# Kernel tuning notes

Measured on AMD Instinct MI355X. Metric: run time of the kernel, lower is better.

The kernel has to match this reference:

```python
import jax, jax.numpy as jnp
import numpy as np


def setup_inputs() -> dict:
    key = jax.random.key(0)
    ks = jax.random.split(key, 8)
    B, T, Hh, Ww, C = 4, 1024, 64, 64, 256
    f = lambda k, s: jax.random.normal(k, s, dtype=jnp.float32)
    return {
        "query_row": f(ks[0], (B, T, C)),
        "query_col": f(ks[1], (B, T, C)),
        "key_row": f(ks[2], (B, Hh, Ww, C)),
        "key_col": f(ks[3], (B, Hh, Ww, C)),
        "value": f(ks[4], (B, Hh, Ww, C)),
        "in_proj_weight": f(ks[5], (5 * C, C)) * 0.02,
        "in_proj_bias": jnp.zeros((5 * C,), jnp.float32),
        "out_w": f(ks[6], (C, C)) * 0.02,
        "out_b": jnp.zeros((C,), jnp.float32),
        "lin_w": f(ks[7], (C, C)) * 0.02,
        "lin_b": jnp.zeros((C,), jnp.float32),
        "num_heads": 8,
    }


def reference(query_row, query_col, key_row, key_col, value,
              in_proj_weight, in_proj_bias, out_w, out_b, lin_w, lin_b,
              num_heads):
    B, T, C = query_row.shape
    Hh, Ww = key_col.shape[1], key_row.shape[2]
    nh = num_heads
    hd = C // nh
    scaling = float(hd) ** -0.5
    W5 = in_proj_weight.reshape(5, C, C)
    b5 = in_proj_bias.reshape(5, C)
    # pooled sigmoid gate over value: AdaptiveAvgPool2d(1) == mean over H,W
    v_avg = jax.nn.sigmoid(value.mean(axis=(1, 2)) @ lin_w.T + lin_b)  # [B, C]
    q_row = (query_row @ W5[0].T + b5[0]) * scaling                    # [B, T, C]
    q_col = (query_col @ W5[1].T + b5[1]) * scaling                    # [B, T, C]
    k_row = (key_row @ W5[2].T + b5[2]).mean(axis=1) * v_avg[:, None, :]  # [B, W, C]
    k_col = (key_col @ W5[3].T + b5[3]).mean(axis=2) * v_avg[:, None, :]  # [B, H, C]
    v = value @ W5[4].T + b5[4]                                        # [B, H, W, C]
    # split heads (C -> nh*hd, same layout as torch view)
    qr = q_row.reshape(B, T, nh, hd)
    qc = q_col.reshape(B, T, nh, hd)
    kr = k_row.reshape(B, Ww, nh, hd)
    kc = k_col.reshape(B, Hh, nh, hd)
    vh = v.reshape(B, Hh, Ww, nh, hd)
    attn_row = jax.nn.softmax(jnp.einsum('btnd,bwnd->bntw', qr, kr), axis=-1)  # [B,nh,T,W]
    attn_col = jax.nn.softmax(jnp.einsum('btnd,bhnd->bnth', qc, kc), axis=-1)  # [B,nh,T,H]
    # column attention over rows of v, then row attention combines
    out_col = jnp.einsum('bnth,bhwnd->bntwd', attn_col, vh)            # [B,nh,T,W,hd]
    out = jnp.einsum('bntw,bntwd->btnd', attn_row, out_col).reshape(B, T, C)
    attn_output = (out @ out_w.T + out_b).transpose(1, 0, 2)           # [T, B, C]
    # head-averaged outer-product attention map [T, B, H, W]
    grid = jnp.einsum('bntw,bnth->tbhw', attn_row, attn_col) / nh
    return attn_output, grid
```

## Files before the change

kernel.cpp:

```cpp
#include <hip/hip_runtime.h>
#include <hip/hip_bf16.h>
#include <math.h>

using bf16x8 = __attribute__((ext_vector_type(8))) short;
using f32x4  = __attribute__((ext_vector_type(4))) float;
using s16x4  = __attribute__((ext_vector_type(4))) short;

static __device__ __forceinline__ float sigmoidf_(float x){ return 1.f/(1.f+__expf(-x)); }
static __device__ __forceinline__ unsigned f2bfu(float f){
  union { float f; unsigned u; } x; x.f = f;
  return (x.u + 0x7FFFu + ((x.u>>16)&1u)) >> 16;
}
static __device__ __forceinline__ short f2bf(float f){ return (short)f2bfu(f); }
static __device__ __forceinline__ unsigned pack2bf(float lo, float hi){
  __hip_bfloat162 h = __float22bfloat162_rn(make_float2(lo, hi));
  unsigned r; __builtin_memcpy(&r, &h, 4);
  return r;
}
static __device__ __forceinline__ float b2f_lo(unsigned u){ union{unsigned u; float f;}x; x.u = u<<16; return x.f; }
static __device__ __forceinline__ float b2f_hi(unsigned u){ union{unsigned u; float f;}x; x.u = u & 0xFFFF0000u; return x.f; }

__device__ __forceinline__ void mfma_body(short* As, short* Bs,
    const float* __restrict__ X, const float* __restrict__ Wm,
    const float* __restrict__ bias, float* __restrict__ Y,
    int bxm, int bxn, float scale, int mode){
  int tid = threadIdx.x;
  int m0 = bxm*128, n0 = bxn*128;
  int l = tid&63, wid = tid>>6, lo16 = l&15, g = l>>4;
  int wm = wid>>1, wn = wid&1;
  f32x4 acc[4][4] = {};
  int srow = tid>>1, skq = (tid&1)*32;
  size_t arow;
  int vb_ = 0, vw0 = 0;
  if (mode==4){
    vb_ = bxm>>5; vw0 = (bxm&31)*2;
    arow = (size_t)(vb_*4096 + (srow&63)*64 + vw0 + (srow>>6));
  } else arow = (size_t)(m0+srow);
  const float4* sa = (const float4*)(X + arow*256 + skq);
  const float4* sb = (const float4*)(Wm + (size_t)(n0+srow)*256 + skq);
  int4* da = (int4*)&As[srow*72 + skq];
  int4* db = (int4*)&Bs[srow*72 + skq];
  for (int k0=0;k0<4;k0++){
    __syncthreads();
    #pragma unroll
    for (int j=0;j<4;j++){
      float4 v0 = sa[2*j], v1 = sa[2*j+1];
      int4 wv;
      wv.x = (int)pack2bf(v0.x, v0.y); wv.y = (int)pack2bf(v0.z, v0.w);
      wv.z = (int)pack2bf(v1.x, v1.y); wv.w = (int)pack2bf(v1.z, v1.w);
      da[j] = wv;
      float4 u0 = sb[2*j], u1 = sb[2*j+1];
      int4 xv;
      xv.x = (int)pack2bf(u0.x, u0.y); xv.y = (int)pack2bf(u0.z, u0.w);
      xv.z = (int)pack2bf(u1.x, u1.y); xv.w = (int)pack2bf(u1.z, u1.w);
      db[j] = xv;
    }
    sa += 16; sb += 16;
    __syncthreads();
    bf16x8 af[4][2], bfr[4][2];
    #pragma unroll
    for (int mt=0;mt<4;mt++)
      #pragma unroll
      for (int c=0;c<2;c++)
        af[mt][c] = *(const bf16x8*)&As[(wm*64 + mt*16 + lo16)*72 + c*32 + g*8];
    #pragma unroll
    for (int nt=0;nt<4;nt++)
      #pragma unroll
      for (int c=0;c<2;c++)
        bfr[nt][c] = *(const bf16x8*)&Bs[(wn*64 + nt*16 + lo16)*72 + c*32 + g*8];
    #pragma unroll
    for (int mt=0;mt<4;mt++)
      #pragma unroll
      for (int nt=0;nt<4;nt++){
        acc[mt][nt] = __builtin_amdgcn_mfma_f32_16x16x32_bf16(af[mt][0], bfr[nt][0], acc[mt][nt], 0,0,0);
        acc[mt][nt] = __builtin_amdgcn_mfma_f32_16x16x32_bf16(af[mt][1], bfr[nt][1], acc[mt][nt], 0,0,0);
      }
  }
  if (mode==4){
    short* vdst = (short*)Y;
    int w = vw0 + wm;
    #pragma unroll
    for (int nt=0;nt<4;nt++){
      int col = n0 + wn*64 + nt*16 + lo16;
      float bv = bias[col];
      int n = col>>5, d = col&31;
      size_t base = (size_t)(vb_*8+n)*131072 + (size_t)w*2048 + d*64;
      #pragma unroll
      for (int mt=0;mt<4;mt++){
        int h0 = mt*16 + g*4;
        s16x4 s;
        #pragma unroll
        for (int r=0;r<4;r++) s[r] = f2bf(acc[mt][nt][r] + bv);
        *(s16x4*)(vdst + base + h0) = s;
      }
    }
  } else if (mode==3){
    #pragma unroll
    for (int nt=0;nt<4;nt++){
      int col = n0 + wn*64 + nt*16 + lo16;
      float bv = bias[col];
      #pragma unroll
      for (int mt=0;mt<4;mt++){
        int row = m0 + wm*64 + mt*16 + g*4;
        #pragma unroll
        for (int r=0;r<4;r++){
          int rr = row + r;
          Y[((size_t)((rr&1023)*4 + (rr>>10)))*256 + col] = acc[mt][nt][r] + bv;
        }
      }
    }
  } else {
    #pragma unroll
    for (int nt=0;nt<4;nt++){
      int col = n0 + wn*64 + nt*16 + lo16;
      float bv = bias[col];
      #pragma unroll
      for (int mt=0;mt<4;mt++){
        int row = m0 + wm*64 + mt*16 + g*4;
        #pragma unroll
        for (int r=0;r<4;r++){
          float y = acc[mt][nt][r] + bv;
          if (mode==0) y *= scale;
          Y[(size_t)(row+r)*256 + col] = y;
        }
      }
    }
  }
}

__device__ __forceinline__ void krkc_body(char* smem,
    const float* __restrict__ krm, const float* __restrict__ kcm,
    const float* __restrict__ ipw, const float* __restrict__ ipb,
    const float* __restrict__ vpart, const float* __restrict__ lin_w,
    const float* __restrict__ lin_b,
    float* __restrict__ kr, float* __restrict__ kc,
    int b, int ny, int z){
  const float* X; const float* Wm; const float* bias; float* Y;
  if (z==0){ X=krm; Wm=ipw+131072; bias=ipb+512; Y=kr; }
  else     { X=kcm; Wm=ipw+196608; bias=ipb+768; Y=kc; }
  float* Ast = (float*)smem;
  float* Bst = (float*)(smem + 8704);
  float* va  = (float*)(smem + 17408);
  float* gsh = (float*)(smem + 18432);
  int tid = threadIdx.x;
  int tx = tid&15, ty = tid>>4;
  int m0 = b*64, n0 = ny*64;
  {
    float s = 0.f;
    #pragma unroll
    for (int i=0;i<32;i++) s += vpart[(size_t)(b*32+i)*256 + tid];
    va[tid] = s * (1.f/4096.f);
  }
  __syncthreads();
  {
    int j = tid>>2, kq = tid&3;
    const float* wrow = lin_w + (size_t)(n0+j)*256 + kq*64;
    const float* vap  = va + kq*64;
    float part = 0.f;
    #pragma unroll
    for (int k=0;k<64;k++) part += vap[k]*wrow[k];
    part += __shfl_xor(part, 1);
    part += __shfl_xor(part, 2);
    if (kq==0) gsh[j] = sigmoidf_(part + lin_b[n0+j]);
  }
  float acc[4][4];
  #pragma unroll
  for (int i=0;i<4;i++)
    #pragma unroll
    for (int j=0;j<4;j++) acc[i][j] = 0.f;

  for (int k0=0;k0<256;k0+=32){
    __syncthreads();
    #pragma unroll
    for (int p=0;p<2;p++){
      int pos = tid + p*256;
      int r = pos>>3, kq = pos&7;
      float4 xa = *(const float4*)&X[(size_t)(m0+r)*256 + k0 + kq*4];
      Ast[(kq*4+0)*68+r]=xa.x; Ast[(kq*4+1)*68+r]=xa.y;
      Ast[(kq*4+2)*68+r]=xa.z; Ast[(kq*4+3)*68+r]=xa.w;
      float4 wb = *(const float4*)&Wm[(size_t)(n0+r)*256 + k0 + kq*4];
      Bst[(kq*4+0)*68+r]=wb.x; Bst[(kq*4+1)*68+r]=wb.y;
      Bst[(kq*4+2)*68+r]=wb.z; Bst[(kq*4+3)*68+r]=wb.w;
    }
    __syncthreads();
    #pragma unroll
    for (int k=0;k<32;k++){
      float4 a  = *(const float4*)&Ast[k*68 + ty*4];
      float4 bv = *(const float4*)&Bst[k*68 + tx*4];
      acc[0][0]+=a.x*bv.x; acc[0][1]+=a.x*bv.y; acc[0][2]+=a.x*bv.z; acc[0][3]+=a.x*bv.w;
      acc[1][0]+=a.y*bv.x; acc[1][1]+=a.y*bv.y; acc[1][2]+=a.y*bv.z; acc[1][3]+=a.y*bv.w;
      acc[2][0]+=a.z*bv.x; acc[2][1]+=a.z*bv.y; acc[2][2]+=a.z*bv.z; acc[2][3]+=a.z*bv.w;
      acc[3][0]+=a.w*bv.x; acc[3][1]+=a.w*bv.y; acc[3][2]+=a.w*bv.z; acc[3][3]+=a.w*bv.w;
    }
  }
  float4 b4 = *(const float4*)&bias[n0 + tx*4];
  float4 g4 = *(const float4*)&gsh[tx*4];
  #pragma unroll
  for (int i=0;i<4;i++){
    int row = m0 + ty*4 + i;
    float4 y = make_float4((acc[i][0]+b4.x)*g4.x, (acc[i][1]+b4.y)*g4.y,
                           (acc[i][2]+b4.z)*g4.z, (acc[i][3]+b4.w)*g4.w);
    *(float4*)&Y[(size_t)row*256 + n0 + tx*4] = y;
  }
}

__global__ __launch_bounds__(256) void k_reduce(
    const float* __restrict__ value, const float* __restrict__ key_row,
    const float* __restrict__ key_col, float* __restrict__ vpart,
    float* __restrict__ krm, float* __restrict__ kcm){
  __shared__ float red[1024];
  int bx = blockIdx.x, c = threadIdx.x;
  int cq = c & 63, rg = c >> 6;
  float4 s4 = make_float4(0.f,0.f,0.f,0.f);
  float oscale; float* outp_; size_t obase;
  if (bx < 128){
    int b = bx >> 5, chunk = bx & 31;
    const float4* p = (const float4*)(value + ((size_t)(b*4096 + chunk*128 + rg))*256) + cq;
    #pragma unroll 8
    for (int i=0;i<32;i++){
      float4 v = p[(size_t)i*256];
      s4.x+=v.x; s4.y+=v.y; s4.z+=v.z; s4.w+=v.w;
    }
    oscale = 1.f; outp_ = vpart; obase = (size_t)bx*256;
  } else if (bx < 384){
    int idx = bx - 128;
    int b = idx >> 6, w = idx & 63;
    const float4* p = (const float4*)(key_row + ((size_t)(b*4096 + w))*256) + cq;
    #pragma unroll 8
    for (int i=0;i<16;i++){
      float4 v = p[(size_t)(rg + 4*i)*4096];
      s4.x+=v.x; s4.y+=v.y; s4.z+=v.z; s4.w+=v.w;
    }
    oscale = 1.f/64.f; outp_ = krm; obase = (size_t)idx*256;
  } else {
    int idx = bx - 384;
    int b = idx >> 6, h = idx & 63;
    const float4* p = (const float4*)(key_col + ((size_t)((b*64+h)*64))*256) + cq;
    #pragma unroll 8
    for (int i=0;i<16;i++){
      float4 v = p[(size_t)(rg + 4*i)*64];
      s4.x+=v.x; s4.y+=v.y; s4.z+=v.z; s4.w+=v.w;
    }
    oscale = 1.f/64.f; outp_ = kcm; obase = (size_t)idx*256;
  }
  *(float4*)&red[rg*256 + cq*4] = s4;
  __syncthreads();
  if (c < 64){
    float4 a0 = *(float4*)&red[c*4];
    float4 a1 = *(float4*)&red[256 + c*4];
    float4 a2 = *(float4*)&red[512 + c*4];
    float4 a3 = *(float4*)&red[768 + c*4];
    float4 o = make_float4((a0.x+a1.x+a2.x+a3.x)*oscale, (a0.y+a1.y+a2.y+a3.y)*oscale,
                           (a0.z+a1.z+a2.z+a3.z)*oscale, (a0.w+a1.w+a2.w+a3.w)*oscale);
    *(float4*)&outp_[obase + c*4] = o;
  }
}

__global__ __launch_bounds__(256) void k_proj(
    const float* __restrict__ krm, const float* __restrict__ kcm,
    const float* __restrict__ value,
    const float* __restrict__ query_row, const float* __restrict__ query_col,
    const float* __restrict__ ipw, const float* __restrict__ ipb,
    const float* __restrict__ vpart, const float* __restrict__ lin_w,
    const float* __restrict__ lin_b,
    float* __restrict__ kr, float* __restrict__ kc,
    float* __restrict__ qr, float* __restrict__ qc,
    short* __restrict__ vpB, float scaling){
  __shared__ __align__(16) char smem[36864];
  int bx = blockIdx.x;
  if (bx < 32){
    int z = bx>>4, rem = bx&15, b = rem&3, ny = rem>>2;
    krkc_body(smem, krm, kcm, ipw, ipb, vpart, lin_w, lin_b, kr, kc, b, ny, z);
    return;
  }
  short* As = (short*)smem;
  short* Bs = (short*)(smem + 18432);
  if (bx < 160){
    int bxx = bx - 32;
    int zz = bxx>>6, rem = bxx&63;
    mfma_body(As, Bs, zz ? query_col : query_row, ipw + (zz?65536:0), ipb + (zz?256:0),
              zz ? qc : qr, rem&31, rem>>5, scaling, 0);
  } else {
    int bxx = bx - 160;
    mfma_body(As, Bs, value, ipw+262144, ipb+1024, (float*)vpB, bxx&127, bxx>>7, 1.f, 4);
  }
}

__global__ void k_attn(const float* __restrict__ qr, const float* __restrict__ kr,
                       const float* __restrict__ qc, const float* __restrict__ kc,
                       short* __restrict__ arB, short* __restrict__ acB){
  int lane = threadIdx.x;
  int tblk = blockIdx.x, n = blockIdx.y, z = blockIdx.z;
  int isCol = z >> 2, b = z & 3;
  const float* q  = isCol ? qc : qr;
  const float* kk = isCol ? kc : kr;
  short* dst = isCol ? acB : arB;
  int bn = b*8 + n;
  float4 kreg[8];
  const float4* kp = (const float4*)(kk + ((size_t)(b*64 + lane))*256 + n*32);
  #pragma unroll
  for (int i=0;i<8;i++) kreg[i] = kp[i];
  size_t qbase = ((size_t)(b*1024) + tblk*16)*256 + n*32;
  for (int i=0;i<16;i+=2){
    const float4* qp0 = (const float4*)(q + qbase + (size_t)i*256);
    const float4* qp1 = (const float4*)(q + qbase + (size_t)(i+1)*256);
    float s0 = 0.f, s1 = 0.f;
    #pragma unroll
    for (int j=0;j<8;j++){
      float4 a = qp0[j], c = qp1[j];
      s0 += a.x*kreg[j].x + a.y*kreg[j].y + a.z*kreg[j].z + a.w*kreg[j].w;
      s1 += c.x*kreg[j].x + c.y*kreg[j].y + c.z*kreg[j].z + c.w*kreg[j].w;
    }
    float e0 = __expf(s0), e1 = __expf(s1);
    float sm0 = e0, sm1 = e1;
    #pragma unroll
    for (int off=32; off; off>>=1){
      sm0 += __shfl_xor(sm0, off);
      sm1 += __shfl_xor(sm1, off);
    }
    size_t off_ = ((size_t)bn*1024 + tblk*16 + i)*64 + lane;
    dst[off_]      = f2bf(e0 / sm0);
    dst[off_ + 64] = f2bf(e1 / sm1);
  }
}

__global__ __launch_bounds__(256) void k_core3(
    const short* __restrict__ acB, const short* __restrict__ arB,
    const __hip_bfloat16* __restrict__ vpB, float* __restrict__ outp){
  __shared__ float ARs[64*36];
  __shared__ float P[4][32*34];
  int tid = threadIdx.x;
  int bn = blockIdx.x, tt = blockIdx.y;
  int b = bn>>3, n = bn&7;
  int t0 = tt*32;

  {
    int w = tid&63, tg = (tid>>6)*8;
    const unsigned short* src = (const unsigned short*)arB + ((size_t)bn*1024 + t0 + tg)*64 + w;
    #pragma unroll
    for (int k=0;k<8;k++)
      ARs[w*36 + tg + k] = b2f_lo((unsigned)src[(size_t)k*64]);
  }

  int l = tid&63, wid = tid>>6, lo16 = l&15, g = l>>4, g4 = g*4;
  bf16x8 af[2][2];
  {
    const short* ab = acB + ((size_t)bn*1024 + t0 + lo16)*64 + g*8;
    #pragma unroll
    for (int ts=0; ts<2; ts++){
      af[ts][0] = *(const bf16x8*)(ab + ts*1024);
      af[ts][1] = *(const bf16x8*)(ab + ts*1024 + 32);
    }
  }
  __syncthreads();

  const short* vb = (const short*)vpB + (size_t)bn*131072 + (size_t)wid*32768 + lo16*64 + g*8;
  bf16x8 ring[4][4];
  #pragma unroll
  for (int s=0;s<4;s++){
    const short* p = vb + (size_t)s*2048;
    ring[s][0] = *(const bf16x8*)(p);
    ring[s][1] = *(const bf16x8*)(p + 32);
    ring[s][2] = *(const bf16x8*)(p + 1024);
    ring[s][3] = *(const bf16x8*)(p + 1056);
  }
  f32x4 o[2][2] = {};
  const f32x4 zz = {0.f,0.f,0.f,0.f};
  int wbase = wid*16;

  #pragma unroll
  for (int wi=0; wi<16; ++wi){
    const int slot = wi & 3;
    bf16x8 c0=ring[slot][0], c1=ring[slot][1], c2=ring[slot][2], c3=ring[slot][3];
    const short* pn = vb + (size_t)((wi+4)&15)*2048;
    ring[slot][0] = *(const bf16x8*)(pn);
    ring[slot][1] = *(const bf16x8*)(pn + 32);
    ring[slot][2] = *(const bf16x8*)(pn + 1024);
    ring[slot][3] = *(const bf16x8*)(pn + 1056);
    int wg = wbase + wi;
    #pragma unroll
    for (int ts=0; ts<2; ts++){
      f32x4 mlo = __builtin_amdgcn_mfma_f32_16x16x32_bf16(af[ts][0], c0, zz, 0,0,0);
      mlo = __builtin_amdgcn_mfma_f32_16x16x32_bf16(af[ts][1], c1, mlo, 0,0,0);
      f32x4 mhi = __builtin_amdgcn_mfma_f32_16x16x32_bf16(af[ts][0], c2, zz, 0,0,0);
      mhi = __builtin_amdgcn_mfma_f32_16x16x32_bf16(af[ts][1], c3, mhi, 0,0,0);
      f32x4 ar4 = *(const f32x4*)&ARs[wg*36 + ts*16 + g4];
      #pragma unroll
      for (int r=0;r<4;r++){ o[ts][0][r] += ar4[r]*mlo[r]; o[ts][1][r] += ar4[r]*mhi[r]; }
    }
  }

  #pragma unroll
  for (int ts=0; ts<2; ts++)
    #pragma unroll
    for (int dh=0; dh<2; dh++)
      #pragma unroll
      for (int r=0;r<4;r++)
        P[wid][(ts*16 + g4 + r)*34 + dh*16 + lo16] = o[ts][dh][r];
  __syncthreads();

  float* obase = outp + ((size_t)b*1024 + t0)*256 + n*32;
  #pragma unroll
  for (int k=0;k<4;k++){
    int idx = k*256 + tid;
    int t = idx>>5, d = idx&31;
    float s = P[0][t*34+d] + P[1][t*34+d] + P[2][t*34+d] + P[3][t*34+d];
    obase[(size_t)t*256 + d] = s;
  }
}

__global__ __launch_bounds__(256) void k_fat2(
    const float* __restrict__ outp, const float* __restrict__ out_w,
    const float* __restrict__ out_b, float* __restrict__ out,
    const short* __restrict__ acB, const short* __restrict__ arB,
    float* __restrict__ gout){
  __shared__ __align__(16) char smem[36864];
  int bx = blockIdx.x;
  if (bx < 64){
    short* As = (short*)smem;
    short* Bs = (short*)(smem + 18432);
    mfma_body(As, Bs, outp, out_w, out_b, out, bx&31, bx>>5, 1.f, 3);
    return;
  }
  float* acs = (float*)smem;
  float* ars = (float*)(smem + 8192);
  int bxx = bx - 64;
  int tid = threadIdx.x, tg = bxx&255, b = bxx>>8;
  int t0 = tg*4;
  {
    int idx = tid*8;
    int n = idx>>8, t = (idx>>6)&3, x = idx&63;
    size_t soff = ((size_t)(b*8+n)*1024 + t0+t)*64 + x;
    uint4 av = *(const uint4*)(acB + soff);
    float* ad = &acs[(n*4+t)*64 + x];
    ad[0]=b2f_lo(av.x); ad[1]=b2f_hi(av.x); ad[2]=b2f_lo(av.y); ad[3]=b2f_hi(av.y);
    ad[4]=b2f_lo(av.z); ad[5]=b2f_hi(av.z); ad[6]=b2f_lo(av.w); ad[7]=b2f_hi(av.w);
    uint4 rv = *(const uint4*)(arB + soff);
    float* rd = &ars[(n*4+t)*64 + x];
    rd[0]=b2f_lo(rv.x); rd[1]=b2f_hi(rv.x); rd[2]=b2f_lo(rv.y); rd[3]=b2f_hi(rv.y);
    rd[4]=b2f_lo(rv.z); rd[5]=b2f_hi(rv.z); rd[6]=b2f_lo(rv.w); rd[7]=b2f_hi(rv.w);
  }
  __syncthreads();
  int t_ = tid>>6, l = tid&63;
  int wg = l&3, hsel = l>>2;
  float acc[4][16];
  #pragma unroll
  for (int i=0;i<4;i++)
    #pragma unroll
    for (int j=0;j<16;j++) acc[i][j] = 0.f;
  #pragma unroll
  for (int n=0;n<8;n++){
    float4 a4 = *(const float4*)&acs[(n*4+t_)*64 + hsel*4];
    const float4* rb = (const float4*)&ars[(n*4+t_)*64 + wg*16];
    float4 r0 = rb[0], r1 = rb[1], r2 = rb[2], r3 = rb[3];
    float rr[16] = {r0.x,r0.y,r0.z,r0.w, r1.x,r1.y,r1.z,r1.w,
                    r2.x,r2.y,r2.z,r2.w, r3.x,r3.y,r3.z,r3.w};
    float aa[4] = {a4.x, a4.y, a4.z, a4.w};
    #pragma unroll
    for (int i=0;i<4;i++)
      #pragma unroll
      for (int j=0;j<16;j++) acc[i][j] += aa[i]*rr[j];
  }
  const float inv = 0.125f;
  float* dstbase = gout + ((size_t)(t0+t_)*4 + b)*4096;
  #pragma unroll
  for (int i=0;i<4;i++){
    float* dst = dstbase + (hsel*4+i)*64 + wg*16;
    #pragma unroll
    for (int jq=0;jq<4;jq++)
      *(float4*)&dst[jq*4] = make_float4(acc[i][jq*4]*inv, acc[i][jq*4+1]*inv,
                                         acc[i][jq*4+2]*inv, acc[i][jq*4+3]*inv);
  }
}

extern "C" void kernel_launch(void* const* d_in, const int* in_sizes, int n_in,
                              void* d_out, int out_size, void* d_ws, size_t ws_size,
                              hipStream_t stream){
  const float* query_row = (const float*)d_in[0];
  const float* query_col = (const float*)d_in[1];
  const float* key_row   = (const float*)d_in[2];
  const float* key_col   = (const float*)d_in[3];
  const float* value     = (const float*)d_in[4];
  const float* ipw       = (const float*)d_in[5];
  const float* ipb       = (const float*)d_in[6];
  const float* out_w     = (const float*)d_in[7];
  const float* out_b     = (const float*)d_in[8];
  const float* lin_w     = (const float*)d_in[9];
  const float* lin_b     = (const float*)d_in[10];
  float* out = (float*)d_out;
  float* ws  = (float*)d_ws;

  float* vpart = ws;
  float* krm   = ws + 32768;
  float* kcm   = ws + 98304;
  float* kr    = ws + 163840;
  float* kc    = ws + 229376;
  float* qr    = ws + 294912;
  float* qc    = ws + 1343488;
  __hip_bfloat16* vpB = (__hip_bfloat16*)(ws + 2392064);
  short* arB  = (short*)(ws + 4489216);
  short* acB  = (short*)(ws + 5537792);
  float* outp = ws + 6586368;

  const float scaling = 0.17677669529663687f;

  hipLaunchKernelGGL(k_reduce, dim3(640), dim3(256), 0, stream,
                     value, key_row, key_col, vpart, krm, kcm);

  hipLaunchKernelGGL(k_proj, dim3(416), dim3(256), 0, stream,
                     krm, kcm, value, query_row, query_col, ipw, ipb,
                     vpart, lin_w, lin_b, kr, kc, qr, qc, (short*)vpB, scaling);

  hipLaunchKernelGGL(k_attn, dim3(64,8,8), dim3(64), 0, stream,
                     qr, kr, qc, kc, arB, acB);

  hipLaunchKernelGGL(k_core3, dim3(32,32), dim3(256), 0, stream, acB, arB, vpB, outp);

  hipLaunchKernelGGL(k_fat2, dim3(1088), dim3(256), 0, stream,
                     outp, out_w, out_b, out, acB, arB, out + 1048576);
}
```

Baseline: 116.1 us.

## Fold key-row/col projection into reduce kernel and apply gate inside attention

The key_row/key_col mean-pooled projections (GEMV per row) are now computed in k_reduce right after the pooling, instead of in 32 SIMT-GEMM blocks inside k_proj. The sigmoid gate becomes a separate tiny computation (4 blocks) in k_proj, and its multiply is applied when k_attn loads keys into registers. k_attn is also repacked to four waves per block. This shortens the critical path of k_proj's slow krkc blocks, at the cost of each reduce block re-reading a 256x256 weight matrix from cache.

Measured after the change: 133.2 us. 1.15x slower.

```diff
diff --git a/kernel.cpp b/kernel.cpp
--- a/kernel.cpp
+++ b/kernel.cpp
@@ -128,91 +128,16 @@
   }
 }
 
-__device__ __forceinline__ void krkc_body(char* smem,
-    const float* __restrict__ krm, const float* __restrict__ kcm,
-    const float* __restrict__ ipw, const float* __restrict__ ipb,
-    const float* __restrict__ vpart, const float* __restrict__ lin_w,
-    const float* __restrict__ lin_b,
-    float* __restrict__ kr, float* __restrict__ kc,
-    int b, int ny, int z){
-  const float* X; const float* Wm; const float* bias; float* Y;
-  if (z==0){ X=krm; Wm=ipw+131072; bias=ipb+512; Y=kr; }
-  else     { X=kcm; Wm=ipw+196608; bias=ipb+768; Y=kc; }
-  float* Ast = (float*)smem;
-  float* Bst = (float*)(smem + 8704);
-  float* va  = (float*)(smem + 17408);
-  float* gsh = (float*)(smem + 18432);
-  int tid = threadIdx.x;
-  int tx = tid&15, ty = tid>>4;
-  int m0 = b*64, n0 = ny*64;
-  {
-    float s = 0.f;
-    #pragma unroll
-    for (int i=0;i<32;i++) s += vpart[(size_t)(b*32+i)*256 + tid];
-    va[tid] = s * (1.f/4096.f);
-  }
-  __syncthreads();
-  {
-    int j = tid>>2, kq = tid&3;
-    const float* wrow = lin_w + (size_t)(n0+j)*256 + kq*64;
-    const float* vap  = va + kq*64;
-    float part = 0.f;
-    #pragma unroll
-    for (int k=0;k<64;k++) part += vap[k]*wrow[k];
-    part += __shfl_xor(part, 1);
-    part += __shfl_xor(part, 2);
-    if (kq==0) gsh[j] = sigmoidf_(part + lin_b[n0+j]);
-  }
-  float acc[4][4];
-  #pragma unroll
-  for (int i=0;i<4;i++)
-    #pragma unroll
-    for (int j=0;j<4;j++) acc[i][j] = 0.f;
-
-  for (int k0=0;k0<256;k0+=32){
-    __syncthreads();
-    #pragma unroll
-    for (int p=0;p<2;p++){
-      int pos = tid + p*256;
-      int r = pos>>3, kq = pos&7;
-      float4 xa = *(const float4*)&X[(size_t)(m0+r)*256 + k0 + kq*4];
-      Ast[(kq*4+0)*68+r]=xa.x; Ast[(kq*4+1)*68+r]=xa.y;
-      Ast[(kq*4+2)*68+r]=xa.z; Ast[(kq*4+3)*68+r]=xa.w;
-      float4 wb = *(const float4*)&Wm[(size_t)(n0+r)*256 + k0 + kq*4];
-      Bst[(kq*4+0)*68+r]=wb.x; Bst[(kq*4+1)*68+r]=wb.y;
-      Bst[(kq*4+2)*68+r]=wb.z; Bst[(kq*4+3)*68+r]=wb.w;
-    }
-    __syncthreads();
-    #pragma unroll
-    for (int k=0;k<32;k++){
-      float4 a  = *(const float4*)&Ast[k*68 + ty*4];
-      float4 bv = *(const float4*)&Bst[k*68 + tx*4];
-      acc[0][0]+=a.x*bv.x; acc[0][1]+=a.x*bv.y; acc[0][2]+=a.x*bv.z; acc[0][3]+=a.x*bv.w;
-      acc[1][0]+=a.y*bv.x; acc[1][1]+=a.y*bv.y; acc[1][2]+=a.y*bv.z; acc[1][3]+=a.y*bv.w;
-      acc[2][0]+=a.z*bv.x; acc[2][1]+=a.z*bv.y; acc[2][2]+=a.z*bv.z; acc[2][3]+=a.z*bv.w;
-      acc[3][0]+=a.w*bv.x; acc[3][1]+=a.w*bv.y; acc[3][2]+=a.w*bv.z; acc[3][3]+=a.w*bv.w;
-    }
-  }
-  float4 b4 = *(const float4*)&bias[n0 + tx*4];
-  float4 g4 = *(const float4*)&gsh[tx*4];
-  #pragma unroll
-  for (int i=0;i<4;i++){
-    int row = m0 + ty*4 + i;
-    float4 y = make_float4((acc[i][0]+b4.x)*g4.x, (acc[i][1]+b4.y)*g4.y,
-                           (acc[i][2]+b4.z)*g4.z, (acc[i][3]+b4.w)*g4.w);
-    *(float4*)&Y[(size_t)row*256 + n0 + tx*4] = y;
-  }
-}
-
 __global__ __launch_bounds__(256) void k_reduce(
     const float* __restrict__ value, const float* __restrict__ key_row,
-    const float* __restrict__ key_col, float* __restrict__ vpart,
-    float* __restrict__ krm, float* __restrict__ kcm){
+    const float* __restrict__ key_col, const float* __restrict__ ipw,
+    const float* __restrict__ ipb,
+    float* __restrict__ vpart, float* __restrict__ kr0, float* __restrict__ kc0){
   __shared__ float red[1024];
+  __shared__ float row[256];
   int bx = blockIdx.x, c = threadIdx.x;
   int cq = c & 63, rg = c >> 6;
   float4 s4 = make_float4(0.f,0.f,0.f,0.f);
-  float oscale; float* outp_; size_t obase;
   if (bx < 128){
     int b = bx >> 5, chunk = bx & 31;
     const float4* p = (const float4*)(value + ((size_t)(b*4096 + chunk*128 + rg))*256) + cq;
@@ -221,9 +146,22 @@
       float4 v = p[(size_t)i*256];
       s4.x+=v.x; s4.y+=v.y; s4.z+=v.z; s4.w+=v.w;
     }
-    oscale = 1.f; outp_ = vpart; obase = (size_t)bx*256;
-  } else if (bx < 384){
-    int idx = bx - 128;
+    *(float4*)&red[rg*256 + cq*4] = s4;
+    __syncthreads();
+    if (c < 64){
+      float4 a0 = *(float4*)&red[c*4];
+      float4 a1 = *(float4*)&red[256 + c*4];
+      float4 a2 = *(float4*)&red[512 + c*4];
+      float4 a3 = *(float4*)&red[768 + c*4];
+      *(float4*)&vpart[(size_t)bx*256 + c*4] =
+        make_float4(a0.x+a1.x+a2.x+a3.x, a0.y+a1.y+a2.y+a3.y,
+                    a0.z+a1.z+a2.z+a3.z, a0.w+a1.w+a2.w+a3.w);
+    }
+    return;
+  }
+  const float* Wm; const float* bias; float* Y; int idx;
+  if (bx < 384){
+    idx = bx - 128;
     int b = idx >> 6, w = idx & 63;
     const float4* p = (const float4*)(key_row + ((size_t)(b*4096 + w))*256) + cq;
     #pragma unroll 8
@@ -231,9 +169,9 @@
       float4 v = p[(size_t)(rg + 4*i)*4096];
       s4.x+=v.x; s4.y+=v.y; s4.z+=v.z; s4.w+=v.w;
     }
-    oscale = 1.f/64.f; outp_ = krm; obase = (size_t)idx*256;
+    Wm = ipw + 131072; bias = ipb + 512; Y = kr0;
   } else {
-    int idx = bx - 384;
+    idx = bx - 384;
     int b = idx >> 6, h = idx & 63;
     const float4* p = (const float4*)(key_col + ((size_t)((b*64+h)*64))*256) + cq;
     #pragma unroll 8
@@ -241,7 +179,7 @@
       float4 v = p[(size_t)(rg + 4*i)*64];
       s4.x+=v.x; s4.y+=v.y; s4.z+=v.z; s4.w+=v.w;
     }
-    oscale = 1.f/64.f; outp_ = kcm; obase = (size_t)idx*256;
+    Wm = ipw + 196608; bias = ipb + 768; Y = kc0;
   }
   *(float4*)&red[rg*256 + cq*4] = s4;
   __syncthreads();
@@ -250,56 +188,91 @@
     float4 a1 = *(float4*)&red[256 + c*4];
     float4 a2 = *(float4*)&red[512 + c*4];
     float4 a3 = *(float4*)&red[768 + c*4];
-    float4 o = make_float4((a0.x+a1.x+a2.x+a3.x)*oscale, (a0.y+a1.y+a2.y+a3.y)*oscale,
-                           (a0.z+a1.z+a2.z+a3.z)*oscale, (a0.w+a1.w+a2.w+a3.w)*oscale);
-    *(float4*)&outp_[obase + c*4] = o;
+    const float inv = 1.f/64.f;
+    *(float4*)&row[c*4] =
+      make_float4((a0.x+a1.x+a2.x+a3.x)*inv, (a0.y+a1.y+a2.y+a3.y)*inv,
+                  (a0.z+a1.z+a2.z+a3.z)*inv, (a0.w+a1.w+a2.w+a3.w)*inv);
+  }
+  __syncthreads();
+  {
+    const float4* wr = (const float4*)(Wm + (size_t)c*256);
+    const float4* rv = (const float4*)row;
+    float acc = bias[c];
+    #pragma unroll 8
+    for (int k=0;k<64;k++){
+      float4 w4 = wr[k]; float4 v4 = rv[k];
+      acc += w4.x*v4.x + w4.y*v4.y + w4.z*v4.z + w4.w*v4.w;
+    }
+    Y[(size_t)idx*256 + c] = acc;
   }
 }
 
 __global__ __launch_bounds__(256) void k_proj(
-    const float* __restrict__ krm, const float* __restrict__ kcm,
     const float* __restrict__ value,
     const float* __restrict__ query_row, const float* __restrict__ query_col,
     const float* __restrict__ ipw, const float* __restrict__ ipb,
     const float* __restrict__ vpart, const float* __restrict__ lin_w,
     const float* __restrict__ lin_b,
-    float* __restrict__ kr, float* __restrict__ kc,
+    float* __restrict__ gate,
     float* __restrict__ qr, float* __restrict__ qc,
     short* __restrict__ vpB, float scaling){
   __shared__ __align__(16) char smem[36864];
   int bx = blockIdx.x;
-  if (bx < 32){
-    int z = bx>>4, rem = bx&15, b = rem&3, ny = rem>>2;
-    krkc_body(smem, krm, kcm, ipw, ipb, vpart, lin_w, lin_b, kr, kc, b, ny, z);
+  if (bx < 4){
+    float* va = (float*)smem;
+    int b = bx, c = threadIdx.x;
+    float s = 0.f;
+    #pragma unroll
+    for (int i=0;i<32;i++) s += vpart[(size_t)(b*32+i)*256 + c];
+    va[c] = s * (1.f/4096.f);
+    __syncthreads();
+    const float4* wr  = (const float4*)(lin_w + (size_t)c*256);
+    const float4* vp4 = (const float4*)va;
+    float acc = lin_b[c];
+    #pragma unroll 8
+    for (int k=0;k<64;k++){
+      float4 w4 = wr[k]; float4 v4 = vp4[k];
+      acc += w4.x*v4.x + w4.y*v4.y + w4.z*v4.z + w4.w*v4.w;
+    }
+    gate[b*256+c] = sigmoidf_(acc);
     return;
   }
   short* As = (short*)smem;
   short* Bs = (short*)(smem + 18432);
-  if (bx < 160){
-    int bxx = bx - 32;
+  if (bx < 132){
+    int bxx = bx - 4;
     int zz = bxx>>6, rem = bxx&63;
     mfma_body(As, Bs, zz ? query_col : query_row, ipw + (zz?65536:0), ipb + (zz?256:0),
               zz ? qc : qr, rem&31, rem>>5, scaling, 0);
   } else {
-    int bxx = bx - 160;
+    int bxx = bx - 132;
     mfma_body(As, Bs, value, ipw+262144, ipb+1024, (float*)vpB, bxx&127, bxx>>7, 1.f, 4);
   }
 }
 
-__global__ void k_attn(const float* __restrict__ qr, const float* __restrict__ kr,
-                       const float* __restrict__ qc, const float* __restrict__ kc,
-                       short* __restrict__ arB, short* __restrict__ acB){
-  int lane = threadIdx.x;
-  int tblk = blockIdx.x, n = blockIdx.y, z = blockIdx.z;
+__global__ __launch_bounds__(256) void k_attn(
+    const float* __restrict__ qr, const float* __restrict__ kr0,
+    const float* __restrict__ qc, const float* __restrict__ kc0,
+    const float* __restrict__ gate,
+    short* __restrict__ arB, short* __restrict__ acB){
+  int tid = threadIdx.x;
+  int lane = tid & 63, wave = tid >> 6;
+  int tblk = blockIdx.x*4 + wave, n = blockIdx.y, z = blockIdx.z;
   int isCol = z >> 2, b = z & 3;
   const float* q  = isCol ? qc : qr;
-  const float* kk = isCol ? kc : kr;
+  const float* kk = isCol ? kc0 : kr0;
   short* dst = isCol ? acB : arB;
   int bn = b*8 + n;
   float4 kreg[8];
-  const float4* kp = (const float4*)(kk + ((size_t)(b*64 + lane))*256 + n*32);
-  #pragma unroll
-  for (int i=0;i<8;i++) kreg[i] = kp[i];
+  {
+    const float4* kp = (const float4*)(kk + ((size_t)(b*64 + lane))*256 + n*32);
+    const float4* gp = (const float4*)(gate + (size_t)b*256 + n*32);
+    #pragma unroll
+    for (int i=0;i<8;i++){
+      float4 kv = kp[i], gv = gp[i];
+      kreg[i] = make_float4(kv.x*gv.x, kv.y*gv.y, kv.z*gv.z, kv.w*gv.w);
+    }
+  }
   size_t qbase = ((size_t)(b*1024) + tblk*16)*256 + n*32;
   for (int i=0;i<16;i+=2){
     const float4* qp0 = (const float4*)(q + qbase + (size_t)i*256);
@@ -491,28 +464,27 @@
   float* ws  = (float*)d_ws;
 
   float* vpart = ws;
-  float* krm   = ws + 32768;
-  float* kcm   = ws + 98304;
-  float* kr    = ws + 163840;
-  float* kc    = ws + 229376;
-  float* qr    = ws + 294912;
-  float* qc    = ws + 1343488;
-  __hip_bfloat16* vpB = (__hip_bfloat16*)(ws + 2392064);
-  short* arB  = (short*)(ws + 4489216);
-  short* acB  = (short*)(ws + 5537792);
-  float* outp = ws + 6586368;
+  float* gate  = ws + 32768;
+  float* kr0   = ws + 33792;
+  float* kc0   = ws + 99328;
+  float* qr    = ws + 164864;
+  float* qc    = ws + 1213440;
+  __hip_bfloat16* vpB = (__hip_bfloat16*)(ws + 2262016);
+  short* arB  = (short*)(ws + 4359168);
+  short* acB  = (short*)(ws + 5407744);
+  float* outp = ws + 6456320;
 
   const float scaling = 0.17677669529663687f;
 
   hipLaunchKernelGGL(k_reduce, dim3(640), dim3(256), 0, stream,
-                     value, key_row, key_col, vpart, krm, kcm);
-
-  hipLaunchKernelGGL(k_proj, dim3(416), dim3(256), 0, stream,
-                     krm, kcm, value, query_row, query_col, ipw, ipb,
-                     vpart, lin_w, lin_b, kr, kc, qr, qc, (short*)vpB, scaling);
-
-  hipLaunchKernelGGL(k_attn, dim3(64,8,8), dim3(64), 0, stream,
-                     qr, kr, qc, kc, arB, acB);
+                     value, key_row, key_col, ipw, ipb, vpart, kr0, kc0);
+
+  hipLaunchKernelGGL(k_proj, dim3(388), dim3(256), 0, stream,
+                     value, query_row, query_col, ipw, ipb,
+                     vpart, lin_w, lin_b, gate, qr, qc, (short*)vpB, scaling);
+
+  hipLaunchKernelGGL(k_attn, dim3(16,8,8), dim3(256), 0, stream,
+                     qr, kr0, qc, kc0, gate, arB, acB);
 
   hipLaunchKernelGGL(k_core3, dim3(32,32), dim3(256), 0, stream, acB, arB, vpB, outp);
 
```

## Compute sigmoid gate once and apply it in attention key load

Applied to the files above, without the earlier changes.

Moves the pooled sigmoid gate computation out of the 32 krkc blocks, which each recomputed a gate slice, into 4 dedicated blocks that write a gate buffer. Attention kernels then multiply the keys by the gate when loading them into registers. This removes redundant gate work and a barrier from the key projection blocks. The attention kernel is also regrouped from 64-thread blocks to 256-thread blocks holding four waves. The added cost is an extra workspace buffer and a gate load per attention wave.

Result: slower. 123.1 us (+6.1%).

```diff
diff --git a/kernel.cpp b/kernel.cpp
--- a/kernel.cpp
+++ b/kernel.cpp
@@ -131,8 +131,6 @@
 __device__ __forceinline__ void krkc_body(char* smem,
     const float* __restrict__ krm, const float* __restrict__ kcm,
     const float* __restrict__ ipw, const float* __restrict__ ipb,
-    const float* __restrict__ vpart, const float* __restrict__ lin_w,
-    const float* __restrict__ lin_b,
     float* __restrict__ kr, float* __restrict__ kc,
     int b, int ny, int z){
   const float* X; const float* Wm; const float* bias; float* Y;
@@ -140,29 +138,9 @@
   else     { X=kcm; Wm=ipw+196608; bias=ipb+768; Y=kc; }
   float* Ast = (float*)smem;
   float* Bst = (float*)(smem + 8704);
-  float* va  = (float*)(smem + 17408);
-  float* gsh = (float*)(smem + 18432);
   int tid = threadIdx.x;
   int tx = tid&15, ty = tid>>4;
   int m0 = b*64, n0 = ny*64;
-  {
-    float s = 0.f;
-    #pragma unroll
-    for (int i=0;i<32;i++) s += vpart[(size_t)(b*32+i)*256 + tid];
-    va[tid] = s * (1.f/4096.f);
-  }
-  __syncthreads();
-  {
-    int j = tid>>2, kq = tid&3;
-    const float* wrow = lin_w + (size_t)(n0+j)*256 + kq*64;
-    const float* vap  = va + kq*64;
-    float part = 0.f;
-    #pragma unroll
-    for (int k=0;k<64;k++) part += vap[k]*wrow[k];
-    part += __shfl_xor(part, 1);
-    part += __shfl_xor(part, 2);
-    if (kq==0) gsh[j] = sigmoidf_(part + lin_b[n0+j]);
-  }
   float acc[4][4];
   #pragma unroll
   for (int i=0;i<4;i++)
@@ -194,12 +172,10 @@
     }
   }
   float4 b4 = *(const float4*)&bias[n0 + tx*4];
-  float4 g4 = *(const float4*)&gsh[tx*4];
   #pragma unroll
   for (int i=0;i<4;i++){
     int row = m0 + ty*4 + i;
-    float4 y = make_float4((acc[i][0]+b4.x)*g4.x, (acc[i][1]+b4.y)*g4.y,
-                           (acc[i][2]+b4.z)*g4.z, (acc[i][3]+b4.w)*g4.w);
+    float4 y = make_float4(acc[i][0]+b4.x, acc[i][1]+b4.y, acc[i][2]+b4.z, acc[i][3]+b4.w);
     *(float4*)&Y[(size_t)row*256 + n0 + tx*4] = y;
   }
 }
@@ -263,43 +239,73 @@
     const float* __restrict__ ipw, const float* __restrict__ ipb,
     const float* __restrict__ vpart, const float* __restrict__ lin_w,
     const float* __restrict__ lin_b,
+    float* __restrict__ gate,
     float* __restrict__ kr, float* __restrict__ kc,
     float* __restrict__ qr, float* __restrict__ qc,
     short* __restrict__ vpB, float scaling){
   __shared__ __align__(16) char smem[36864];
   int bx = blockIdx.x;
-  if (bx < 32){
-    int z = bx>>4, rem = bx&15, b = rem&3, ny = rem>>2;
-    krkc_body(smem, krm, kcm, ipw, ipb, vpart, lin_w, lin_b, kr, kc, b, ny, z);
+  if (bx < 4){
+    float* va = (float*)smem;
+    int b = bx, c = threadIdx.x;
+    float s = 0.f;
+    #pragma unroll
+    for (int i=0;i<32;i++) s += vpart[(size_t)(b*32+i)*256 + c];
+    va[c] = s * (1.f/4096.f);
+    __syncthreads();
+    const float4* wr  = (const float4*)(lin_w + (size_t)c*256);
+    const float4* vp4 = (const float4*)va;
+    float acc = lin_b[c];
+    #pragma unroll 8
+    for (int k=0;k<64;k++){
+      float4 w4 = wr[k]; float4 v4 = vp4[k];
+      acc += w4.x*v4.x + w4.y*v4.y + w4.z*v4.z + w4.w*v4.w;
+    }
+    gate[b*256+c] = sigmoidf_(acc);
+    return;
+  }
+  if (bx < 36){
+    int bxx = bx - 4;
+    int z = bxx>>4, rem = bxx&15, b = rem&3, ny = rem>>2;
+    krkc_body(smem, krm, kcm, ipw, ipb, kr, kc, b, ny, z);
     return;
   }
   short* As = (short*)smem;
   short* Bs = (short*)(smem + 18432);
-  if (bx < 160){
-    int bxx = bx - 32;
+  if (bx < 164){
+    int bxx = bx - 36;
     int zz = bxx>>6, rem = bxx&63;
     mfma_body(As, Bs, zz ? query_col : query_row, ipw + (zz?65536:0), ipb + (zz?256:0),
               zz ? qc : qr, rem&31, rem>>5, scaling, 0);
   } else {
-    int bxx = bx - 160;
+    int bxx = bx - 164;
     mfma_body(As, Bs, value, ipw+262144, ipb+1024, (float*)vpB, bxx&127, bxx>>7, 1.f, 4);
   }
 }
 
-__global__ void k_attn(const float* __restrict__ qr, const float* __restrict__ kr,
-                       const float* __restrict__ qc, const float* __restrict__ kc,
-                       short* __restrict__ arB, short* __restrict__ acB){
-  int lane = threadIdx.x;
-  int tblk = blockIdx.x, n = blockIdx.y, z = blockIdx.z;
+__global__ __launch_bounds__(256) void k_attn(
+    const float* __restrict__ qr, const float* __restrict__ kr0,
+    const float* __restrict__ qc, const float* __restrict__ kc0,
+    const float* __restrict__ gate,
+    short* __restrict__ arB, short* __restrict__ acB){
+  int tid = threadIdx.x;
+  int lane = tid & 63, wave = tid >> 6;
+  int tblk = blockIdx.x*4 + wave, n = blockIdx.y, z = blockIdx.z;
   int isCol = z >> 2, b = z & 3;
   const float* q  = isCol ? qc : qr;
-  const float* kk = isCol ? kc : kr;
+  const float* kk = isCol ? kc0 : kr0;
   short* dst = isCol ? acB : arB;
   int bn = b*8 + n;
   float4 kreg[8];
-  const float4* kp = (const float4*)(kk + ((size_t)(b*64 + lane))*256 + n*32);
-  #pragma unroll
-  for (int i=0;i<8;i++) kreg[i] = kp[i];
+  {
+    const float4* kp = (const float4*)(kk + ((size_t)(b*64 + lane))*256 + n*32);
+    const float4* gp = (const float4*)(gate + (size_t)b*256 + n*32);
+    #pragma unroll
+    for (int i=0;i<8;i++){
+      float4 kv = kp[i], gv = gp[i];
+      kreg[i] = make_float4(kv.x*gv.x, kv.y*gv.y, kv.z*gv.z, kv.w*gv.w);
+    }
+  }
   size_t qbase = ((size_t)(b*1024) + tblk*16)*256 + n*32;
   for (int i=0;i<16;i+=2){
     const float4* qp0 = (const float4*)(q + qbase + (size_t)i*256);
@@ -491,28 +497,29 @@
   float* ws  = (float*)d_ws;
 
   float* vpart = ws;
-  float* krm   = ws + 32768;
-  float* kcm   = ws + 98304;
-  float* kr    = ws + 163840;
-  float* kc    = ws + 229376;
-  float* qr    = ws + 294912;
-  float* qc    = ws + 1343488;
-  __hip_bfloat16* vpB = (__hip_bfloat16*)(ws + 2392064);
-  short* arB  = (short*)(ws + 4489216);
-  short* acB  = (short*)(ws + 5537792);
-  float* outp = ws + 6586368;
+  float* gate  = ws + 32768;
+  float* krm   = ws + 33792;
+  float* kcm   = ws + 99328;
+  float* kr0   = ws + 164864;
+  float* kc0   = ws + 230400;
+  float* qr    = ws + 295936;
+  float* qc    = ws + 1344512;
+  __hip_bfloat16* vpB = (__hip_bfloat16*)(ws + 2393088);
+  short* arB  = (short*)(ws + 4490240);
+  short* acB  = (short*)(ws + 5538816);
+  float* outp = ws + 6587392;
 
   const float scaling = 0.17677669529663687f;
 
   hipLaunchKernelGGL(k_reduce, dim3(640), dim3(256), 0, stream,
                      value, key_row, key_col, vpart, krm, kcm);
 
-  hipLaunchKernelGGL(k_proj, dim3(416), dim3(256), 0, stream,
+  hipLaunchKernelGGL(k_proj, dim3(420), dim3(256), 0, stream,
                      krm, kcm, value, query_row, query_col, ipw, ipb,
-                     vpart, lin_w, lin_b, kr, kc, qr, qc, (short*)vpB, scaling);
-
-  hipLaunchKernelGGL(k_attn, dim3(64,8,8), dim3(64), 0, stream,
-                     qr, kr, qc, kc, arB, acB);
+                     vpart, lin_w, lin_b, gate, kr0, kc0, qr, qc, (short*)vpB, scaling);
+
+  hipLaunchKernelGGL(k_attn, dim3(16,8,8), dim3(256), 0, stream,
+                     qr, kr0, qc, kc0, gate, arB, acB);
 
   hipLaunchKernelGGL(k_core3, dim3(32,32), dim3(256), 0, stream, acB, arB, vpB, outp);
 
```
